# Performance work log

Measured on AMD Instinct MI355X. Metric: run time of the kernel, lower is better.

## Reference

```python
import jax, jax.numpy as jnp
import numpy as np

BETA = 0.25  # commitment loss weight


def setup_inputs() -> dict:
    key = jax.random.key(0)
    k1, k2 = jax.random.split(key)
    z = jax.random.normal(k1, (16, 256, 64, 64), dtype=jnp.float32)      # encoder latent, NCHW
    codebook = jax.random.normal(k2, (1024, 256), dtype=jnp.float32)     # [n_e, e_dim]
    return {"z": z, "codebook": codebook}


def reference(z, codebook):
    B, C, H, W = z.shape
    z_bhwc = jnp.transpose(z, (0, 2, 3, 1))            # [B,H,W,C]
    zf = z_bhwc.reshape(-1, C)                          # [N,C], N = B*H*W
    # squared L2 distance to every codeword: ||z||^2 + ||e||^2 - 2 z.e
    d = ((zf * zf).sum(axis=1, keepdims=True)
         + (codebook * codebook).sum(axis=1)[None, :]
         - 2.0 * zf @ codebook.T)                       # [N, n_e]
    idx = jnp.argmin(d, axis=1)                         # [N] nearest codeword
    zq = codebook[idx].reshape(B, H, W, C)              # irregular gather
    # VQ loss: codebook term + beta * commitment term
    loss = (BETA * jnp.mean((jax.lax.stop_gradient(zq) - z_bhwc) ** 2)
            + jnp.mean((zq - jax.lax.stop_gradient(z_bhwc)) ** 2))
    # straight-through estimator
    zq_st = z_bhwc + jax.lax.stop_gradient(zq - z_bhwc)
    return jnp.transpose(zq_st, (0, 3, 1, 2)), loss
```

## Files before the change

kernel.cpp:

```cpp
#include <hip/hip_runtime.h>
#include <cfloat>

#define C_DIM 256
#define HW    4096
#define NE    1024
#define NPIX  65536
#define TAU   0.15f
#define ZSTR  264

typedef __attribute__((ext_vector_type(8))) _Float16 half8_t;
typedef __attribute__((ext_vector_type(4))) float floatx4;

__device__ __forceinline__ unsigned int fenc(float f) {
  unsigned int u = __float_as_uint(f);
  return (u & 0x80000000u) ? ~u : (u | 0x80000000u);
}


__global__ __launch_bounds__(256)
void prep_kernel(const float* __restrict__ cb, _Float16* __restrict__ EhfP,
                 float* __restrict__ e2) {
  if (blockIdx.x < 128) {
    const int g = blockIdx.x >> 3, it = blockIdx.x & 7;
    const int sidx = it * 256 + (int)threadIdx.x;
    const int ks = sidx >> 8, i = (sidx >> 6) & 3, lane = sidx & 63;
    const int ln = lane & 15, quad = lane >> 4;
    const float* src = cb + (size_t)(g * 64 + i * 16 + ln) * C_DIM + ks * 32 + quad * 8;
    const float4 v0 = *(const float4*)(src);
    const float4 v1 = *(const float4*)(src + 4);
    half8_t h;
    h[0] = (_Float16)v0.x; h[1] = (_Float16)v0.y; h[2] = (_Float16)v0.z; h[3] = (_Float16)v0.w;
    h[4] = (_Float16)v1.x; h[5] = (_Float16)v1.y; h[6] = (_Float16)v1.z; h[7] = (_Float16)v1.w;
    *(half8_t*)(EhfP + (size_t)g * 16384 + (size_t)sidx * 8) = h;
  } else {
    const int bid = blockIdx.x - 128;
    const int wave = (bid * 256 + (int)threadIdx.x) >> 6;
    const int lane = threadIdx.x & 63;
    const float4 v = *(const float4*)(cb + (size_t)wave * C_DIM + lane * 4);
    float s = v.x * v.x + v.y * v.y + v.z * v.z + v.w * v.w;
    #pragma unroll
    for (int off = 32; off; off >>= 1) s += __shfl_down(s, off, 64);
    if (lane == 0) e2[wave] = s;
  }
}

__global__ __launch_bounds__(256, 2)
void screen_kernel(const float* __restrict__ z, const _Float16* __restrict__ EhfP,
                   const float* __restrict__ e2, int* __restrict__ idx_out,
                   int* __restrict__ clist, int* __restrict__ ccount,
                   float* __restrict__ acc_out) {
  __shared__ __align__(16) _Float16 Zl[128 * ZSTR];
  __shared__ float e2l[NE];

  const int tid = threadIdx.x;
  const int ptile = blockIdx.x * 128;
  const int b = ptile >> 12, pb = ptile & 4095;
  const float* zb = z + (size_t)b * (C_DIM * HW) + pb;

  float s_z2 = 0.f;
  #pragma unroll
  for (int it = 0; it < 16; ++it) {
    const int flat = it * 256 + tid;
    const int p = flat & 127, kb = flat >> 7;
    float f[8];
    #pragma unroll
    for (int j = 0; j < 8; ++j) f[j] = zb[(size_t)(kb * 8 + j) * HW + p];
    half8_t h;
    #pragma unroll
    for (int j = 0; j < 8; ++j) { s_z2 = fmaf(f[j], f[j], s_z2); h[j] = (_Float16)f[j]; }
    *(half8_t*)&Zl[p * ZSTR + kb * 8] = h;
  }
  #pragma unroll
  for (int i = 0; i < 4; ++i) e2l[i * 256 + tid] = e2[i * 256 + tid];
  __syncthreads();

  const int lane = tid & 63;
  const int w = tid >> 6;
  const int wc = w & 1, wp = w >> 1;
  const int ln = lane & 15, quad = lane >> 4;

  const _Float16* aBase = EhfP + (size_t)wc * 16384 + (size_t)lane * 8;
  const char* rowB[4];
  #pragma unroll
  for (int j = 0; j < 4; ++j)
    rowB[j] = (const char*)(&Zl[(wp * 64 + j * 16 + ln) * ZSTR + quad * 8]);

  float d1[4], d2[4]; int i1[4];
  #pragma unroll
  for (int j = 0; j < 4; ++j) { d1[j] = FLT_MAX; d2[j] = FLT_MAX; i1[j] = 0; }

  half8_t abuf[2][4], bbuf[2][4];
  #pragma unroll
  for (int i = 0; i < 4; ++i) abuf[0][i] = *(const half8_t*)(aBase + i * 512);
  #pragma unroll
  for (int j = 0; j < 4; ++j) bbuf[0][j] = *(const half8_t*)(rowB[j]);

  for (int nc = 0; nc < 8; ++nc) {
    floatx4 acc[4][4];
    #pragma unroll
    for (int i = 0; i < 4; ++i)
      #pragma unroll
      for (int j = 0; j < 4; ++j) acc[i][j] = (floatx4){0.f, 0.f, 0.f, 0.f};

    #pragma unroll
    for (int ks = 0; ks < 8; ++ks) {
      const int cur = ks & 1, nxt = cur ^ 1;
      const int s1 = nc * 8 + ks + 1;
      const int sp = s1 > 63 ? 63 : s1;
      const size_t aoff = (size_t)(sp >> 3) * 32768 + (size_t)(sp & 7) * 2048;
      const int bks = sp & 7;
      #pragma unroll
      for (int i = 0; i < 4; ++i) abuf[nxt][i] = *(const half8_t*)(aBase + aoff + i * 512);
      #pragma unroll
      for (int j = 0; j < 4; ++j) bbuf[nxt][j] = *(const half8_t*)(rowB[j] + bks * 64);
      #pragma unroll
      for (int i = 0; i < 4; ++i)
        #pragma unroll
        for (int j = 0; j < 4; ++j)
          acc[i][j] = __builtin_amdgcn_mfma_f32_16x16x32_f16(abuf[cur][i], bbuf[cur][j], acc[i][j], 0, 0, 0);
    }

    const int cwb = nc * 128 + wc * 64;
    #pragma unroll
    for (int i = 0; i < 4; ++i) {
      const int cw0 = cwb + i * 16 + quad * 4;
      float ee[4];
      #pragma unroll
      for (int r = 0; r < 4; ++r) ee[r] = e2l[cw0 + r];
      #pragma unroll
      for (int j = 0; j < 4; ++j) {
        #pragma unroll
        for (int r = 0; r < 4; ++r) {
          const float d = fmaf(-2.0f, acc[i][j][r], ee[r]);
          const bool lt = d < d1[j];
          const float hi = lt ? d1[j] : d;
          d1[j] = lt ? d : d1[j];
          i1[j] = lt ? (cw0 + r) : i1[j];
          d2[j] = fminf(d2[j], hi);
        }
      }
    }
  }

  #pragma unroll
  for (int j = 0; j < 4; ++j) {
    #pragma unroll
    for (int m = 16; m <= 32; m <<= 1) {
      const float od1 = __shfl_xor(d1[j], m, 64);
      const int   oi1 = __shfl_xor(i1[j], m, 64);
      const float od2 = __shfl_xor(d2[j], m, 64);
      const bool take = (od1 < d1[j]) || (od1 == d1[j] && oi1 < i1[j]);
      const float hi = take ? d1[j] : od1;
      d1[j] = take ? od1 : d1[j];
      i1[j] = take ? oi1 : i1[j];
      d2[j] = fminf(fminf(d2[j], od2), hi);
    }
  }

  __syncthreads();
  float* rd1  = (float*)Zl;
  int*   ri1  = (int*)Zl + 256;
  float* rd2  = (float*)Zl + 512;
  float* zsq  = (float*)Zl + 768;
  float* dsum = (float*)Zl + 1024;
  if (lane < 16) {
    #pragma unroll
    for (int j = 0; j < 4; ++j) {
      const int p = wp * 64 + j * 16 + ln;
      rd1[wc * 128 + p] = d1[j];
      ri1[wc * 128 + p] = i1[j];
      rd2[wc * 128 + p] = d2[j];
    }
  }
  zsq[tid] = s_z2;
  __syncthreads();
  if (tid < 128) {
    const float a1 = rd1[tid], b1 = rd1[128 + tid];
    const int   ai = ri1[tid], bi = ri1[128 + tid];
    const float a2 = rd2[tid], b2 = rd2[128 + tid];
    const bool take = (b1 < a1) || (b1 == a1 && bi < ai);
    const float d1f = take ? b1 : a1;
    const int   i1f = take ? bi : ai;
    const float hi  = take ? a1 : b1;
    const float d2f = fminf(fminf(a2, b2), hi);
    const int gp = ptile + tid;
    idx_out[gp] = i1f;
    dsum[tid] = d1f;
    if ((d2f - d1f) <= TAU) {
      const int pos = atomicAdd(ccount, 1);
      clist[pos] = gp;
    }
  }
  __syncthreads();
  if (tid < 64) {
    float v = zsq[tid] + zsq[tid + 64] + zsq[tid + 128] + zsq[tid + 192]
            + dsum[tid] + dsum[tid + 64];
    #pragma unroll
    for (int off = 32; off; off >>= 1) v += __shfl_down(v, off, 64);
    if (tid == 0) atomicAdd(acc_out, v);
  }
}

__global__ __launch_bounds__(256)
void rescan_kernel(const float* __restrict__ z, const float* __restrict__ cb,
                   const float* __restrict__ e2, const int* __restrict__ clist,
                   const int* __restrict__ ccount, int* __restrict__ idx_out) {
  __shared__ __align__(16) float zl[4][C_DIM];
  __shared__ int pxs[4];
  __shared__ unsigned long long bestk[4];
  const int n = *ccount;
  const int ngroups = (n + 3) >> 2;
  for (int g = blockIdx.x; g < ngroups; g += gridDim.x) {
    const int base = g * 4;
    if ((int)threadIdx.x < 4) {
      pxs[threadIdx.x] = clist[min(base + (int)threadIdx.x, n - 1)];
      bestk[threadIdx.x] = ~0ULL;
    }
    __syncthreads();
    {
      const int k = threadIdx.x;
      #pragma unroll
      for (int i = 0; i < 4; ++i) {
        const int gp = pxs[i];
        zl[i][k] = z[(size_t)(gp >> 12) * (C_DIM * HW) + (size_t)k * HW + (gp & 4095)];
      }
    }
    __syncthreads();
    unsigned long long mykey[4] = {~0ULL, ~0ULL, ~0ULL, ~0ULL};
    #pragma unroll 1
    for (int o = 0; o < 4; ++o) {
      const int cw = o * 256 + (int)threadIdx.x;
      const float* row = cb + (size_t)cw * C_DIM;
      float dot[4] = {0.f, 0.f, 0.f, 0.f};
      #pragma unroll 4
      for (int k0 = 0; k0 < C_DIM; k0 += 4) {
        const float4 ev = *(const float4*)(row + k0);
        #pragma unroll
        for (int i = 0; i < 4; ++i) {
          const float4 zz = *(const float4*)&zl[i][k0];
          dot[i] = fmaf(ev.x, zz.x, dot[i]);
          dot[i] = fmaf(ev.y, zz.y, dot[i]);
          dot[i] = fmaf(ev.z, zz.z, dot[i]);
          dot[i] = fmaf(ev.w, zz.w, dot[i]);
        }
      }
      const float ee = e2[cw];
      #pragma unroll
      for (int i = 0; i < 4; ++i) {
        const float d = fmaf(-2.0f, dot[i], ee);
        const unsigned long long key = ((unsigned long long)fenc(d) << 32) | (unsigned)cw;
        mykey[i] = key < mykey[i] ? key : mykey[i];
      }
    }
    #pragma unroll
    for (int i = 0; i < 4; ++i) {
      unsigned long long k = mykey[i];
      #pragma unroll
      for (int off = 32; off; off >>= 1) {
        const unsigned long long ok = __shfl_xor(k, off, 64);
        k = ok < k ? ok : k;
      }
      if ((threadIdx.x & 63) == 0) atomicMin(&bestk[i], k);
    }
    __syncthreads();
    if ((int)threadIdx.x < 4)
      idx_out[pxs[threadIdx.x]] = (int)(unsigned)(bestk[threadIdx.x] & 0xFFFFFFFFull);
    __syncthreads();
  }
}

__global__ __launch_bounds__(256)
void scatter_kernel(const float* __restrict__ cb, const int* __restrict__ idx,
                    float* __restrict__ out) {
  const int tid = threadIdx.x;
  const int px = blockIdx.x * 64 + (tid & 63);
  const int cbase = (tid >> 6) * 64;
  const int id = idx[px];
  const int b = px >> 12, p = px & 4095;
  float*       orow = out + (size_t)b * (C_DIM * HW) + p;
  const float* erow = cb + (size_t)id * C_DIM;
  #pragma unroll 4
  for (int c0 = cbase; c0 < cbase + 64; c0 += 4) {
    const float4 ev = *(const float4*)(erow + c0);
    orow[(size_t)(c0 + 0) * HW] = ev.x;
    orow[(size_t)(c0 + 1) * HW] = ev.y;
    orow[(size_t)(c0 + 2) * HW] = ev.z;
    orow[(size_t)(c0 + 3) * HW] = ev.w;
  }
}

__global__ void finalize_kernel(const float* __restrict__ acc, float* __restrict__ loss_out) {
  *loss_out = 1.25f * (*acc) * (1.0f / 16777216.0f);
}

extern "C" void kernel_launch(void* const* d_in, const int* in_sizes, int n_in,
                              void* d_out, int out_size, void* d_ws, size_t ws_size,
                              hipStream_t stream) {
  const float* z  = (const float*)d_in[0];
  const float* cb = (const float*)d_in[1];
  float* out = (float*)d_out;
  char* ws = (char*)d_ws;

  float*    acc    = (float*)ws;
  int*      ccount = (int*)(ws + 8);
  float*    e2     = (float*)(ws + 4096);
  _Float16* EhfP   = (_Float16*)(ws + 8192);
  int*      idx    = (int*)(ws + 532480);
  int*      clist  = (int*)(ws + 794624);

  (void)hipMemsetAsync(d_ws, 0, 16, stream);
  prep_kernel<<<384, 256, 0, stream>>>(cb, EhfP, e2);
  screen_kernel<<<NPIX / 128, 256, 0, stream>>>(z, EhfP, e2, idx, clist, ccount, acc);
  rescan_kernel<<<1024, 256, 0, stream>>>(z, cb, e2, clist, ccount, idx);
  scatter_kernel<<<NPIX / 64, 256, 0, stream>>>(cb, idx, out);
  finalize_kernel<<<1, 1, 0, stream>>>(acc, out + 16777216);
}
```

Before: 222.6 us.

## Fuse codeword scatter into screen and rescan kernels, drop idx buffer

Removes the separate scatter kernel and the global index array. The screen kernel writes the gathered codeword for each pixel straight to the NCHW output. The rescan kernel then overwrites the output rows of ambiguous pixels with the refined codeword. This saves one kernel launch plus the index write and read round trip. In exchange, some pixels' output rows are written twice, and the screen kernel's tail gets longer with store-heavy work at occupancy 2.

```diff
diff --git a/kernel.cpp b/kernel.cpp
--- a/kernel.cpp
+++ b/kernel.cpp
@@ -46,9 +46,9 @@
 
 __global__ __launch_bounds__(256, 2)
 void screen_kernel(const float* __restrict__ z, const _Float16* __restrict__ EhfP,
-                   const float* __restrict__ e2, int* __restrict__ idx_out,
+                   const float* __restrict__ e2, const float* __restrict__ cb,
                    int* __restrict__ clist, int* __restrict__ ccount,
-                   float* __restrict__ acc_out) {
+                   float* __restrict__ acc_out, float* __restrict__ out) {
   __shared__ __align__(16) _Float16 Zl[128 * ZSTR];
   __shared__ float e2l[NE];
 
@@ -163,6 +163,7 @@
   float* rd2  = (float*)Zl + 512;
   float* zsq  = (float*)Zl + 768;
   float* dsum = (float*)Zl + 1024;
+  int*   fid  = (int*)Zl + 1152;
   if (lane < 16) {
     #pragma unroll
     for (int j = 0; j < 4; ++j) {
@@ -183,12 +184,11 @@
     const int   i1f = take ? bi : ai;
     const float hi  = take ? a1 : b1;
     const float d2f = fminf(fminf(a2, b2), hi);
-    const int gp = ptile + tid;
-    idx_out[gp] = i1f;
+    fid[tid]  = i1f;
     dsum[tid] = d1f;
     if ((d2f - d1f) <= TAU) {
       const int pos = atomicAdd(ccount, 1);
-      clist[pos] = gp;
+      clist[pos] = ptile + tid;
     }
   }
   __syncthreads();
@@ -199,12 +199,26 @@
     for (int off = 32; off; off >>= 1) v += __shfl_down(v, off, 64);
     if (tid == 0) atomicAdd(acc_out, v);
   }
+  {
+    const int pl = tid & 127, cs = tid >> 7;
+    const int id = fid[pl];
+    const float* er = cb + (size_t)id * C_DIM + cs * 128;
+    float* orow = out + (size_t)b * (C_DIM * HW) + (size_t)(cs * 128) * HW + pb + pl;
+    #pragma unroll 8
+    for (int c = 0; c < 128; c += 4) {
+      const float4 ev = *(const float4*)(er + c);
+      orow[(size_t)(c + 0) * HW] = ev.x;
+      orow[(size_t)(c + 1) * HW] = ev.y;
+      orow[(size_t)(c + 2) * HW] = ev.z;
+      orow[(size_t)(c + 3) * HW] = ev.w;
+    }
+  }
 }
 
 __global__ __launch_bounds__(256)
 void rescan_kernel(const float* __restrict__ z, const float* __restrict__ cb,
                    const float* __restrict__ e2, const int* __restrict__ clist,
-                   const int* __restrict__ ccount, int* __restrict__ idx_out) {
+                   const int* __restrict__ ccount, float* __restrict__ out) {
   __shared__ __align__(16) float zl[4][C_DIM];
   __shared__ int pxs[4];
   __shared__ unsigned long long bestk[4];
@@ -263,29 +277,20 @@
       if ((threadIdx.x & 63) == 0) atomicMin(&bestk[i], k);
     }
     __syncthreads();
-    if ((int)threadIdx.x < 4)
-      idx_out[pxs[threadIdx.x]] = (int)(unsigned)(bestk[threadIdx.x] & 0xFFFFFFFFull);
+    {
+      const int i = (int)threadIdx.x >> 6;
+      const int l = (int)threadIdx.x & 63;
+      const int gp = pxs[i];
+      const int id = (int)(unsigned)(bestk[i] & 0xFFFFFFFFull);
+      const float* er = cb + (size_t)id * C_DIM;
+      float* orow = out + (size_t)(gp >> 12) * (C_DIM * HW) + (gp & 4095);
+      const float4 ev = *(const float4*)(er + l * 4);
+      orow[(size_t)(l * 4 + 0) * HW] = ev.x;
+      orow[(size_t)(l * 4 + 1) * HW] = ev.y;
+      orow[(size_t)(l * 4 + 2) * HW] = ev.z;
+      orow[(size_t)(l * 4 + 3) * HW] = ev.w;
+    }
     __syncthreads();
-  }
-}
-
-__global__ __launch_bounds__(256)
-void scatter_kernel(const float* __restrict__ cb, const int* __restrict__ idx,
-                    float* __restrict__ out) {
-  const int tid = threadIdx.x;
-  const int px = blockIdx.x * 64 + (tid & 63);
-  const int cbase = (tid >> 6) * 64;
-  const int id = idx[px];
-  const int b = px >> 12, p = px & 4095;
-  float*       orow = out + (size_t)b * (C_DIM * HW) + p;
-  const float* erow = cb + (size_t)id * C_DIM;
-  #pragma unroll 4
-  for (int c0 = cbase; c0 < cbase + 64; c0 += 4) {
-    const float4 ev = *(const float4*)(erow + c0);
-    orow[(size_t)(c0 + 0) * HW] = ev.x;
-    orow[(size_t)(c0 + 1) * HW] = ev.y;
-    orow[(size_t)(c0 + 2) * HW] = ev.z;
-    orow[(size_t)(c0 + 3) * HW] = ev.w;
   }
 }
 
@@ -305,13 +310,11 @@
   int*      ccount = (int*)(ws + 8);
   float*    e2     = (float*)(ws + 4096);
   _Float16* EhfP   = (_Float16*)(ws + 8192);
-  int*      idx    = (int*)(ws + 532480);
-  int*      clist  = (int*)(ws + 794624);
+  int*      clist  = (int*)(ws + 532480);
 
   (void)hipMemsetAsync(d_ws, 0, 16, stream);
   prep_kernel<<<384, 256, 0, stream>>>(cb, EhfP, e2);
-  screen_kernel<<<NPIX / 128, 256, 0, stream>>>(z, EhfP, e2, idx, clist, ccount, acc);
-  rescan_kernel<<<1024, 256, 0, stream>>>(z, cb, e2, clist, ccount, idx);
-  scatter_kernel<<<NPIX / 64, 256, 0, stream>>>(cb, idx, out);
+  screen_kernel<<<NPIX / 128, 256, 0, stream>>>(z, EhfP, e2, cb, clist, ccount, acc, out);
+  rescan_kernel<<<1024, 256, 0, stream>>>(z, cb, e2, clist, ccount, out);
   finalize_kernel<<<1, 1, 0, stream>>>(acc, out + 16777216);
 }
```

Result: faster. 207.7 us (-6.7%).
